# Kernel tuning notes

Hardware: AMD Instinct MI355X
Metric: run time of the kernel (lower is better)

The kernel has to match this reference:

```python
import jax, jax.numpy as jnp
import numpy as np

DEGREE = 3          # polynomial degree -> 2*(DEGREE+1)=8 coeffs per query
S = 16              # sampling_points along the curve
NP = 2              # num_points (offsets per sampling point)
S_SCALE = 0.077     # self.s offset scale
SHAPES = [(100, 100), (50, 50), (25, 25)]   # memory_spatial_shapes
STARTS = [0, 10000, 12500]                  # memory_level_start_index
HID = 256


def _grid_sample(feat, grid):
    """F.grid_sample(mode='bilinear', padding_mode='zeros', align_corners=False).
    feat: [B,C,H,W], grid: [B,Q,S,2] in [-1,1] (x=width, y=height) -> [B,Q,S,C]."""
    B, C, H, W = feat.shape
    x = (grid[..., 0] + 1.0) * (W * 0.5) - 0.5
    y = (grid[..., 1] + 1.0) * (H * 0.5) - 0.5
    x0 = jnp.floor(x); y0 = jnp.floor(y)
    x1 = x0 + 1.0;     y1 = y0 + 1.0
    wx1 = x - x0; wx0 = 1.0 - wx1
    wy1 = y - y0; wy0 = 1.0 - wy1
    feat_t = jnp.transpose(feat, (0, 2, 3, 1))  # [B,H,W,C]
    bidx = jnp.arange(B)[:, None, None]

    def gather(xi, yi):
        valid = (xi >= 0) & (xi < W) & (yi >= 0) & (yi < H)
        xc = jnp.clip(xi, 0, W - 1).astype(jnp.int32)
        yc = jnp.clip(yi, 0, H - 1).astype(jnp.int32)
        v = feat_t[bidx, yc, xc]                 # [B,Q,S,C]
        return v * valid[..., None].astype(feat.dtype)

    return (gather(x0, y0) * (wx0 * wy0)[..., None]
          + gather(x1, y0) * (wx1 * wy0)[..., None]
          + gather(x0, y1) * (wx0 * wy1)[..., None]
          + gather(x1, y1) * (wx1 * wy1)[..., None])


def setup_inputs() -> dict:
    key = jax.random.key(0)
    k1, k2, k3, k4, k5 = jax.random.split(key, 5)
    B, Q = 16, 300
    T = sum(h * w for h, w in SHAPES)
    return {
        "ref_polys": jax.random.uniform(k1, (B, Q, 2 * (DEGREE + 1)), jnp.float32),
        "memory": jax.random.normal(k2, (B, T, HID), jnp.float32),
        "w1": jax.random.normal(k3, (HID, HID), jnp.float32) * (1.0 / np.sqrt(HID)),
        "b1": jnp.zeros((HID,), jnp.float32),
        "w2": jax.random.normal(k4, (HID, 2 * NP), jnp.float32) * (1.0 / np.sqrt(HID)),
        "b2": jnp.zeros((2 * NP,), jnp.float32),
        "ref_levels": jax.random.randint(k5, (B, Q), 0, 3, jnp.int32),
    }


def reference(ref_polys, memory, w1, b1, w2, b2, ref_levels):
    B, Q, _ = ref_polys.shape
    C = memory.shape[-1]
    rp = jax.lax.stop_gradient(ref_polys)  # ref_polys_detach in the original

    # lambdas: [S, DEGREE+1], rows are [t^3, t^2, t, 1]
    t = jnp.linspace(0.0, 1.0, S)
    lam = jnp.stack([t ** i for i in range(DEGREE, -1, -1)], axis=1)

    # poly evaluation -> normalized sampling locations in [-1,1]: [B,Q,S,2]
    sp = 2.0 * (jnp.einsum('bqce,se->bqsc', rp.reshape(B, Q, 2, DEGREE + 1), lam) - 0.5)

    # multi-level bilinear sampling
    embs = []
    for (h, w), st in zip(SHAPES, STARTS):
        feat = jnp.transpose(memory[:, st:st + h * w, :], (0, 2, 1)).reshape(B, C, h, w)
        embs.append(_grid_sample(feat, sp))
    emb = jnp.stack(embs, 1)  # [B, L, Q, S, C]

    # faithful to torch.gather(dim=2) with index [B,1,Q,S,C]:
    # out[b,0,q,s,c] = emb[b,0,ref_levels[b,q],s,c]  (gathers along the QUERY dim of level 0)
    g = emb[:, 0][jnp.arange(B)[:, None], ref_levels]  # [B,Q,S,C]

    # sampler_head MLP (2 layers, tanh activation between)
    h1 = jnp.tanh(g @ w1 + b1)
    off = (h1 @ w2 + b2).reshape(B, Q, S, NP, 2)

    out = S_SCALE * jnp.tanh(off) + sp[:, :, :, None, :]
    return out.reshape(B, Q, S * NP, 2)
```

## Files before the change

kernel.cpp:

```cpp
#include <hip/hip_runtime.h>

#define B_    16
#define Q_    300
#define S_    16
#define HID_  256
#define SSCALE 0.077f

__global__ __launch_bounds__(256) void sample_mlp_kernel(
    const float* __restrict__ ref_polys,
    const float* __restrict__ memory,
    const float* __restrict__ w1,
    const float* __restrict__ b1,
    const float* __restrict__ w2,
    const float* __restrict__ b2,
    float* __restrict__ off_table)
{
    const int blk = blockIdx.x;
    const int s   = blk & 15;
    const int bq  = blk >> 4;
    const int b   = bq / 3;
    const int qi  = bq - b * 3;
    const int tid = threadIdx.x;

    const float* rp = ref_polys + (size_t)(b * Q_ + qi) * 8;
    const float t = (float)s * (1.0f / 15.0f);
    const float px = ((rp[0] * t + rp[1]) * t + rp[2]) * t + rp[3];
    const float py = ((rp[4] * t + rp[5]) * t + rp[6]) * t + rp[7];
    const float spx = 2.0f * px - 1.0f;
    const float spy = 2.0f * py - 1.0f;

    const float x = (spx + 1.0f) * 50.0f - 0.5f;
    const float y = (spy + 1.0f) * 50.0f - 0.5f;
    const float x0f = floorf(x), y0f = floorf(y);
    const int   x0 = (int)x0f,  y0 = (int)y0f;
    const int   x1 = x0 + 1,    y1 = y0 + 1;
    const float wx1 = x - x0f, wx0 = 1.0f - wx1;
    const float wy1 = y - y0f, wy0 = 1.0f - wy1;
    const bool vx0 = (x0 >= 0) & (x0 < 100);
    const bool vx1 = (x1 >= 0) & (x1 < 100);
    const bool vy0 = (y0 >= 0) & (y0 < 100);
    const bool vy1 = (y1 >= 0) & (y1 < 100);
    const int cx0 = min(max(x0, 0), 99), cx1 = min(max(x1, 0), 99);
    const int cy0 = min(max(y0, 0), 99), cy1 = min(max(y1, 0), 99);
    const float w00 = (vx0 && vy0) ? wx0 * wy0 : 0.0f;
    const float w10 = (vx1 && vy0) ? wx1 * wy0 : 0.0f;
    const float w01 = (vx0 && vy1) ? wx0 * wy1 : 0.0f;
    const float w11 = (vx1 && vy1) ? wx1 * wy1 : 0.0f;

    const float* mb  = memory + (size_t)b * 13125 * 256;
    const float* r00 = mb + (size_t)(cy0 * 100 + cx0) * 256;
    const float* r10 = mb + (size_t)(cy0 * 100 + cx1) * 256;
    const float* r01 = mb + (size_t)(cy1 * 100 + cx0) * 256;
    const float* r11 = mb + (size_t)(cy1 * 100 + cx1) * 256;

    __shared__ float gs[HID_];
    __shared__ float h1s[HID_];

    const int c = tid;
    float g = w00 * r00[c] + w10 * r10[c] + w01 * r01[c] + w11 * r11[c];
    gs[c] = g;
    __syncthreads();

    float acc = b1[tid];
    const float* w1c = w1 + tid;
    #pragma unroll 8
    for (int k = 0; k < HID_; ++k) {
        acc += gs[k] * w1c[(size_t)k * HID_];
    }
    h1s[tid] = tanhf(acc);
    __syncthreads();

    if (tid < 64) {
        float p0 = 0.f, p1 = 0.f, p2 = 0.f, p3 = 0.f;
        #pragma unroll
        for (int j = tid; j < HID_; j += 64) {
            const float h = h1s[j];
            const float* w2r = w2 + j * 4;
            p0 += h * w2r[0];
            p1 += h * w2r[1];
            p2 += h * w2r[2];
            p3 += h * w2r[3];
        }
        #pragma unroll
        for (int off = 32; off; off >>= 1) {
            p0 += __shfl_down(p0, off);
            p1 += __shfl_down(p1, off);
            p2 += __shfl_down(p2, off);
            p3 += __shfl_down(p3, off);
        }
        if (tid == 0) {
            float* o = off_table + ((size_t)bq * 16 + s) * 4;
            o[0] = SSCALE * tanhf(p0 + b2[0]);
            o[1] = SSCALE * tanhf(p1 + b2[1]);
            o[2] = SSCALE * tanhf(p2 + b2[2]);
            o[3] = SSCALE * tanhf(p3 + b2[3]);
        }
    }
}

__global__ __launch_bounds__(256) void out_kernel(
    const float* __restrict__ ref_polys,
    const int*   __restrict__ ref_levels,
    const float* __restrict__ off_table,
    float* __restrict__ out)
{
    const int gid  = blockIdx.x * 256 + threadIdx.x;
    const int lane = gid & 63;
    const int w    = gid >> 6;
    const int b    = w / Q_;
    const int s    = lane >> 2;
    const int npc  = lane & 3;
    const int c    = lane & 1;

    const float* rp = ref_polys + (size_t)w * 8 + c * 4;
    const float t  = (float)s * (1.0f / 15.0f);
    const float sp = 2.0f * (((rp[0] * t + rp[1]) * t + rp[2]) * t + rp[3]) - 1.0f;

    const int lvl = ref_levels[w];
    const float off = off_table[(((size_t)b * 3 + lvl) * 16 + s) * 4 + npc];
    out[gid] = off + sp;
}

extern "C" void kernel_launch(void* const* d_in, const int* in_sizes, int n_in,
                              void* d_out, int out_size, void* d_ws, size_t ws_size,
                              hipStream_t stream) {
    const float* ref_polys  = (const float*)d_in[0];
    const float* memory     = (const float*)d_in[1];
    const float* w1         = (const float*)d_in[2];
    const float* b1         = (const float*)d_in[3];
    const float* w2         = (const float*)d_in[4];
    const float* b2         = (const float*)d_in[5];
    const int*   ref_levels = (const int*)d_in[6];
    float* out = (float*)d_out;

    float* off_table = (float*)d_ws;

    sample_mlp_kernel<<<dim3(B_ * 3 * S_), dim3(256), 0, stream>>>(
        ref_polys, memory, w1, b1, w2, b2, off_table);

    const int total = B_ * Q_ * S_ * 2 * 2;
    out_kernel<<<dim3(total / 256), dim3(256), 0, stream>>>(
        ref_polys, ref_levels, off_table, out);
}
```

Measured before the change: 270.0 us.

## Batch four sample points per block to reuse w1 loads, vectorize output writes

The sampling+MLP kernel now handles four sampling points per block instead of one, storing the four gathered feature vectors as float4 in shared memory so each w1 element loaded from global memory feeds four accumulators. The second layer is spread across all four wavefronts, one per sample. The output kernel writes float2 pairs with half as many threads. This cuts w1 traffic fourfold but drops the block count from 768 to 192, which lowers parallelism on a GPU with many CUs.

New measurement: 270.2 us. No clear change (+0.1%).

```diff
diff --git a/kernel.cpp b/kernel.cpp
--- a/kernel.cpp
+++ b/kernel.cpp
@@ -16,85 +16,97 @@
     float* __restrict__ off_table)
 {
     const int blk = blockIdx.x;
-    const int s   = blk & 15;
-    const int bq  = blk >> 4;
+    const int sq  = blk & 3;
+    const int bq  = blk >> 2;
     const int b   = bq / 3;
     const int qi  = bq - b * 3;
     const int tid = threadIdx.x;
 
+    __shared__ float4 gs4[HID_];
+    __shared__ float  h1s[4][HID_];
+
     const float* rp = ref_polys + (size_t)(b * Q_ + qi) * 8;
-    const float t = (float)s * (1.0f / 15.0f);
-    const float px = ((rp[0] * t + rp[1]) * t + rp[2]) * t + rp[3];
-    const float py = ((rp[4] * t + rp[5]) * t + rp[6]) * t + rp[7];
-    const float spx = 2.0f * px - 1.0f;
-    const float spy = 2.0f * py - 1.0f;
+    const float r0 = rp[0], r1 = rp[1], r2 = rp[2], r3 = rp[3];
+    const float r4 = rp[4], r5 = rp[5], r6 = rp[6], r7 = rp[7];
+    const float* mb = memory + (size_t)b * 13125 * 256;
 
-    const float x = (spx + 1.0f) * 50.0f - 0.5f;
-    const float y = (spy + 1.0f) * 50.0f - 0.5f;
-    const float x0f = floorf(x), y0f = floorf(y);
-    const int   x0 = (int)x0f,  y0 = (int)y0f;
-    const int   x1 = x0 + 1,    y1 = y0 + 1;
-    const float wx1 = x - x0f, wx0 = 1.0f - wx1;
-    const float wy1 = y - y0f, wy0 = 1.0f - wy1;
-    const bool vx0 = (x0 >= 0) & (x0 < 100);
-    const bool vx1 = (x1 >= 0) & (x1 < 100);
-    const bool vy0 = (y0 >= 0) & (y0 < 100);
-    const bool vy1 = (y1 >= 0) & (y1 < 100);
-    const int cx0 = min(max(x0, 0), 99), cx1 = min(max(x1, 0), 99);
-    const int cy0 = min(max(y0, 0), 99), cy1 = min(max(y1, 0), 99);
-    const float w00 = (vx0 && vy0) ? wx0 * wy0 : 0.0f;
-    const float w10 = (vx1 && vy0) ? wx1 * wy0 : 0.0f;
-    const float w01 = (vx0 && vy1) ? wx0 * wy1 : 0.0f;
-    const float w11 = (vx1 && vy1) ? wx1 * wy1 : 0.0f;
+    float gv[4];
+    #pragma unroll
+    for (int i = 0; i < 4; ++i) {
+        const int s = sq * 4 + i;
+        const float t = (float)s * (1.0f / 15.0f);
+        const float spx = 2.0f * (((r0 * t + r1) * t + r2) * t + r3) - 1.0f;
+        const float spy = 2.0f * (((r4 * t + r5) * t + r6) * t + r7) - 1.0f;
 
-    const float* mb  = memory + (size_t)b * 13125 * 256;
-    const float* r00 = mb + (size_t)(cy0 * 100 + cx0) * 256;
-    const float* r10 = mb + (size_t)(cy0 * 100 + cx1) * 256;
-    const float* r01 = mb + (size_t)(cy1 * 100 + cx0) * 256;
-    const float* r11 = mb + (size_t)(cy1 * 100 + cx1) * 256;
+        const float x = (spx + 1.0f) * 50.0f - 0.5f;
+        const float y = (spy + 1.0f) * 50.0f - 0.5f;
+        const float x0f = floorf(x), y0f = floorf(y);
+        const int   x0 = (int)x0f,  y0 = (int)y0f;
+        const int   x1 = x0 + 1,    y1 = y0 + 1;
+        const float wx1 = x - x0f, wx0 = 1.0f - wx1;
+        const float wy1 = y - y0f, wy0 = 1.0f - wy1;
+        const bool vx0 = (x0 >= 0) & (x0 < 100);
+        const bool vx1 = (x1 >= 0) & (x1 < 100);
+        const bool vy0 = (y0 >= 0) & (y0 < 100);
+        const bool vy1 = (y1 >= 0) & (y1 < 100);
+        const int cx0 = min(max(x0, 0), 99), cx1 = min(max(x1, 0), 99);
+        const int cy0 = min(max(y0, 0), 99), cy1 = min(max(y1, 0), 99);
+        const float w00 = (vx0 && vy0) ? wx0 * wy0 : 0.0f;
+        const float w10 = (vx1 && vy0) ? wx1 * wy0 : 0.0f;
+        const float w01 = (vx0 && vy1) ? wx0 * wy1 : 0.0f;
+        const float w11 = (vx1 && vy1) ? wx1 * wy1 : 0.0f;
 
-    __shared__ float gs[HID_];
-    __shared__ float h1s[HID_];
-
-    const int c = tid;
-    float g = w00 * r00[c] + w10 * r10[c] + w01 * r01[c] + w11 * r11[c];
-    gs[c] = g;
+        gv[i] = w00 * mb[(size_t)(cy0 * 100 + cx0) * 256 + tid]
+              + w10 * mb[(size_t)(cy0 * 100 + cx1) * 256 + tid]
+              + w01 * mb[(size_t)(cy1 * 100 + cx0) * 256 + tid]
+              + w11 * mb[(size_t)(cy1 * 100 + cx1) * 256 + tid];
+    }
+    gs4[tid] = make_float4(gv[0], gv[1], gv[2], gv[3]);
     __syncthreads();
 
-    float acc = b1[tid];
+    const float bb = b1[tid];
+    float a0 = bb, a1 = bb, a2 = bb, a3 = bb;
     const float* w1c = w1 + tid;
     #pragma unroll 8
     for (int k = 0; k < HID_; ++k) {
-        acc += gs[k] * w1c[(size_t)k * HID_];
+        const float w = w1c[(size_t)k * HID_];
+        const float4 g = gs4[k];
+        a0 += g.x * w;
+        a1 += g.y * w;
+        a2 += g.z * w;
+        a3 += g.w * w;
     }
-    h1s[tid] = tanhf(acc);
+    h1s[0][tid] = tanhf(a0);
+    h1s[1][tid] = tanhf(a1);
+    h1s[2][tid] = tanhf(a2);
+    h1s[3][tid] = tanhf(a3);
     __syncthreads();
 
-    if (tid < 64) {
-        float p0 = 0.f, p1 = 0.f, p2 = 0.f, p3 = 0.f;
-        #pragma unroll
-        for (int j = tid; j < HID_; j += 64) {
-            const float h = h1s[j];
-            const float* w2r = w2 + j * 4;
-            p0 += h * w2r[0];
-            p1 += h * w2r[1];
-            p2 += h * w2r[2];
-            p3 += h * w2r[3];
-        }
-        #pragma unroll
-        for (int off = 32; off; off >>= 1) {
-            p0 += __shfl_down(p0, off);
-            p1 += __shfl_down(p1, off);
-            p2 += __shfl_down(p2, off);
-            p3 += __shfl_down(p3, off);
-        }
-        if (tid == 0) {
-            float* o = off_table + ((size_t)bq * 16 + s) * 4;
-            o[0] = SSCALE * tanhf(p0 + b2[0]);
-            o[1] = SSCALE * tanhf(p1 + b2[1]);
-            o[2] = SSCALE * tanhf(p2 + b2[2]);
-            o[3] = SSCALE * tanhf(p3 + b2[3]);
-        }
+    const int wv = tid >> 6;
+    const int ln = tid & 63;
+    float p0 = 0.f, p1 = 0.f, p2 = 0.f, p3 = 0.f;
+    #pragma unroll
+    for (int j = ln; j < HID_; j += 64) {
+        const float h = h1s[wv][j];
+        const float* w2r = w2 + j * 4;
+        p0 += h * w2r[0];
+        p1 += h * w2r[1];
+        p2 += h * w2r[2];
+        p3 += h * w2r[3];
+    }
+    #pragma unroll
+    for (int off = 32; off; off >>= 1) {
+        p0 += __shfl_down(p0, off);
+        p1 += __shfl_down(p1, off);
+        p2 += __shfl_down(p2, off);
+        p3 += __shfl_down(p3, off);
+    }
+    if (ln == 0) {
+        float* o = off_table + ((size_t)bq * 16 + sq * 4 + wv) * 4;
+        o[0] = SSCALE * tanhf(p0 + b2[0]);
+        o[1] = SSCALE * tanhf(p1 + b2[1]);
+        o[2] = SSCALE * tanhf(p2 + b2[2]);
+        o[3] = SSCALE * tanhf(p3 + b2[3]);
     }
 }
 
@@ -102,23 +114,24 @@
     const float* __restrict__ ref_polys,
     const int*   __restrict__ ref_levels,
     const float* __restrict__ off_table,
-    float* __restrict__ out)
+    float2* __restrict__ out)
 {
-    const int gid  = blockIdx.x * 256 + threadIdx.x;
-    const int lane = gid & 63;
-    const int w    = gid >> 6;
-    const int b    = w / Q_;
-    const int s    = lane >> 2;
-    const int npc  = lane & 3;
-    const int c    = lane & 1;
+    const int t   = blockIdx.x * 256 + threadIdx.x;
+    const int idx = t & 31;
+    const int w   = t >> 5;
+    const int b   = w / Q_;
+    const int s   = idx >> 1;
+    const int np  = idx & 1;
 
-    const float* rp = ref_polys + (size_t)w * 8 + c * 4;
-    const float t  = (float)s * (1.0f / 15.0f);
-    const float sp = 2.0f * (((rp[0] * t + rp[1]) * t + rp[2]) * t + rp[3]) - 1.0f;
+    const float* rp = ref_polys + (size_t)w * 8;
+    const float tt  = (float)s * (1.0f / 15.0f);
+    const float spx = 2.0f * (((rp[0] * tt + rp[1]) * tt + rp[2]) * tt + rp[3]) - 1.0f;
+    const float spy = 2.0f * (((rp[4] * tt + rp[5]) * tt + rp[6]) * tt + rp[7]) - 1.0f;
 
     const int lvl = ref_levels[w];
-    const float off = off_table[(((size_t)b * 3 + lvl) * 16 + s) * 4 + npc];
-    out[gid] = off + sp;
+    const float2 off = *(const float2*)(off_table
+        + (((size_t)b * 3 + lvl) * 16 + s) * 4 + np * 2);
+    out[t] = make_float2(off.x + spx, off.y + spy);
 }
 
 extern "C" void kernel_launch(void* const* d_in, const int* in_sizes, int n_in,
@@ -135,10 +148,9 @@
 
     float* off_table = (float*)d_ws;
 
-    sample_mlp_kernel<<<dim3(B_ * 3 * S_), dim3(256), 0, stream>>>(
+    sample_mlp_kernel<<<dim3(B_ * 3 * (S_ / 4)), dim3(256), 0, stream>>>(
         ref_polys, memory, w1, b1, w2, b2, off_table);
 
-    const int total = B_ * Q_ * S_ * 2 * 2;
-    out_kernel<<<dim3(total / 256), dim3(256), 0, stream>>>(
-        ref_polys, ref_levels, off_table, out);
+    out_kernel<<<dim3(600), dim3(256), 0, stream>>>(
+        ref_polys, ref_levels, off_table, (float2*)out);
 }
```
